# Optimization experiments

Measured on AMD Instinct MI355X. Metric: run time of the kernel, lower is better.

The kernel has to match this reference:

```python
import jax, jax.numpy as jnp
import numpy as np

B, L = 8, 896
D_MODEL, N_HEAD, D_HEAD, D_INNER = 320, 10, 32, 1280
LN_EPS = 1e-5


def layernorm(x, g, b):
    mu = jnp.mean(x, axis=-1, keepdims=True)
    var = jnp.mean(jnp.square(x - mu), axis=-1, keepdims=True)
    return (x - mu) * jax.lax.rsqrt(var + LN_EPS) * g + b


def setup_inputs() -> dict:
    key = jax.random.key(0)
    ks = jax.random.split(key, 8)
    w = lambda k, shape: (jax.random.normal(k, shape, jnp.float32) * 0.02)
    return {
        "Z": jax.random.normal(ks[0], (B, L, D_MODEL), jnp.float32),
        "D": jax.random.uniform(ks[1], (B, L, L), jnp.float32),  # nonneg sq-distance bias
        "new_mask": jnp.zeros((B, L, L), jnp.float32),           # additive mask (0 = keep)
        "mask": jnp.ones((B, L, L), jnp.float32),                # multiplicative validity mask
        "gamma": jnp.ones((4, 4), jnp.float32),
        "w_qkv": w(ks[2], (D_MODEL, 3 * D_MODEL)),
        "b_qkv": jnp.zeros((3 * D_MODEL,), jnp.float32),
        "w_o": w(ks[3], (D_MODEL, D_MODEL)),
        "ln1_g": jnp.ones((D_MODEL,), jnp.float32),
        "ln1_b": jnp.zeros((D_MODEL,), jnp.float32),
        "ln2_g": jnp.ones((D_MODEL,), jnp.float32),
        "ln2_b": jnp.zeros((D_MODEL,), jnp.float32),
        "w1": w(ks[4], (D_MODEL, D_INNER)),
        "b1": jnp.zeros((D_INNER,), jnp.float32),
        "w2": w(ks[5], (D_INNER, D_MODEL)),
        "b2": jnp.zeros((D_MODEL,), jnp.float32),
        "N": 128, "M": 256, "P": 512,
    }


def reference(Z, D, new_mask, mask, gamma, w_qkv, b_qkv, w_o,
              ln1_g, ln1_b, ln2_g, ln2_b, w1, b1, w2, b2, N, M, P):
    bsz, n_elem, _ = Z.shape
    sqrtd = np.sqrt(D_HEAD).astype(np.float32)

    # per-pair type bias: segment ids 0=atom,1=bond,2=triplet (use_quad=False)
    seg = jnp.concatenate([
        jnp.zeros((N,), jnp.int32),
        jnp.ones((M,), jnp.int32),
        jnp.full((P,), 2, jnp.int32),
    ])  # [L]
    gamma_mask = gamma[seg[:, None], seg[None, :]]  # [L, L]

    inp = Z
    Zn = layernorm(Z, ln1_g, ln1_b)
    qkv = (Zn @ w_qkv + b_qkv).reshape(bsz, n_elem, N_HEAD, 3 * D_HEAD)
    Z2, Z3, Z4 = jnp.split(qkv, 3, axis=3)  # each [b, L, h, d]

    # scores [b, h, n, m]
    scores = jnp.einsum('bnhd,bmhd->bhnm', Z3, Z4) / sqrtd
    W = -(gamma_mask[None] * D)[:, None] + scores + new_mask[:, None]
    W = jax.nn.softmax(W, axis=3) * mask[:, None]

    attn_out = jnp.einsum('bhnm,bmhd->bnhd', W, Z2).reshape(bsz, n_elem, D_MODEL)
    attn_out = jax.nn.leaky_relu(attn_out, 0.01) @ w_o  # o_net has no bias
    Z_res = attn_out + inp

    Zn2 = layernorm(Z_res, ln2_g, ln2_b)
    out = jax.nn.relu(Zn2 @ w1 + b1) @ w2 + b2 + Z_res
    return out
```

## Files before the change

kernel.cpp:

```cpp
#include <hip/hip_runtime.h>

#define BB 8
#define LLEN 896
#define DMODEL 320
#define NHEAD 10
#define DHEAD 32
#define DINNER 1280
#define ROWS (BB*LLEN)

typedef float f32x4 __attribute__((ext_vector_type(4)));
typedef float f32x16 __attribute__((ext_vector_type(16)));
typedef __bf16 bf16x8 __attribute__((ext_vector_type(8)));

__device__ __forceinline__ float bf2f(unsigned short u) {
    union { unsigned int i; float f; } x;
    x.i = ((unsigned int)u) << 16;
    return x.f;
}
__device__ __forceinline__ unsigned short f2bf(float f) {
    unsigned int u = __float_as_uint(f);
    u += 0x7FFF + ((u >> 16) & 1);
    return (unsigned short)(u >> 16);
}

#define GLOAD16(g, l)                                                              \
    __builtin_amdgcn_global_load_lds(                                              \
        (const __attribute__((address_space(1))) void*)(g),                        \
        (__attribute__((address_space(3))) void*)(__attribute__((address_space(3))) char*)(l), \
        16, 0, 0)

__global__ __launch_bounds__(256) void transpose_bf16(const float* __restrict__ src,
                                                      unsigned short* __restrict__ dst,
                                                      int R, int C) {
    __shared__ float tile[32][33];
    int c0 = blockIdx.x * 32;
    int r0 = blockIdx.y * 32;
    int tx = threadIdx.x & 31, ty = threadIdx.x >> 5;
#pragma unroll
    for (int k = 0; k < 4; ++k) {
        int yy = ty + 8 * k;
        tile[yy][tx] = src[(size_t)(r0 + yy) * C + c0 + tx];
    }
    __syncthreads();
#pragma unroll
    for (int k = 0; k < 4; ++k) {
        int yy = ty + 8 * k;
        dst[(size_t)(c0 + yy) * R + r0 + tx] = f2bf(tile[tx][yy]);
    }
}

__global__ __launch_bounds__(256) void prepass(const float* __restrict__ D,
                                               const float* __restrict__ nm,
                                               const float* __restrict__ mk,
                                               const float* __restrict__ gamma,
                                               unsigned int* __restrict__ combo) {
    __shared__ unsigned int tile[32][33];
    int mt = blockIdx.x, m0 = mt * 32;
    int n0 = blockIdx.y * 32;
    int b = blockIdx.z;
    int sn = (n0 < 128) ? 0 : (n0 < 384) ? 1 : 2;
    int sm = (m0 < 128) ? 0 : (m0 < 384) ? 1 : 2;
    float g = gamma[sn * 4 + sm];
    int tx = threadIdx.x & 31, ty = threadIdx.x >> 5;
#pragma unroll
    for (int k = 0; k < 4; ++k) {
        int nl = ty + 8 * k;
        size_t idx = ((size_t)b * LLEN + n0 + nl) * LLEN + m0 + tx;
        float bias = -g * D[idx] + nm[idx];
        tile[nl][tx] = (unsigned int)f2bf(bias) | ((unsigned int)f2bf(mk[idx]) << 16);
    }
    __syncthreads();
#pragma unroll
    for (int k = 0; k < 4; ++k) {
        int nl = ty + 8 * k;
        combo[(((size_t)b * 28 + mt) * LLEN + n0 + nl) * 32 + tx] = tile[nl][tx];
    }
}

__global__ __launch_bounds__(256) void vt_kernel(const unsigned short* __restrict__ qkv,
                                                 unsigned short* __restrict__ Vt) {
    __shared__ unsigned short tile[32][33];
    int mt = blockIdx.x, h = blockIdx.y, b = blockIdx.z;
    int tx = threadIdx.x & 31, ty = threadIdx.x >> 5;
#pragma unroll
    for (int k = 0; k < 4; ++k) {
        int ml = ty + 8 * k;
        tile[ml][tx] = qkv[((size_t)(b * LLEN) + mt * 32 + ml) * 960 + h * 96 + tx];
    }
    __syncthreads();
#pragma unroll
    for (int k = 0; k < 4; ++k) {
        int d = ty + 8 * k;
        Vt[(((size_t)b * NHEAD + h) * 32 + d) * LLEN + mt * 32 + tx] = tile[tx][d];
    }
}

__global__ __launch_bounds__(320) void ln_kernel(const float* __restrict__ x,
                                                 const float* __restrict__ g,
                                                 const float* __restrict__ bia,
                                                 unsigned short* __restrict__ y) {
    int row = blockIdx.x;
    int t = threadIdx.x;
    float v = x[(size_t)row * DMODEL + t];
    float s = v;
#pragma unroll
    for (int o = 1; o < 64; o <<= 1) s += __shfl_xor(s, o, 64);
    __shared__ float red[10];
    int w = t >> 6;
    if ((t & 63) == 0) red[w] = s;
    __syncthreads();
    float mu = (red[0] + red[1] + red[2] + red[3] + red[4]) * (1.0f / DMODEL);
    float d = v - mu;
    float s2 = d * d;
#pragma unroll
    for (int o = 1; o < 64; o <<= 1) s2 += __shfl_xor(s2, o, 64);
    if ((t & 63) == 0) red[5 + w] = s2;
    __syncthreads();
    float var = (red[5] + red[6] + red[7] + red[8] + red[9]) * (1.0f / DMODEL);
    float inv = rsqrtf(var + 1e-5f);
    y[(size_t)row * DMODEL + t] = f2bf(d * inv * g[t] + bia[t]);
}

template <int EPI>
__global__ __launch_bounds__(256) void gemm_bt(const unsigned short* __restrict__ A,
                                               const unsigned short* __restrict__ BT,
                                               const float* __restrict__ bias,
                                               const float* __restrict__ resid,
                                               void* __restrict__ outv,
                                               int M, int N, int K) {
    __shared__ unsigned short As[2][128][64];
    __shared__ unsigned short Bs[2][64][64];
    int tid = threadIdx.x;
    int m0 = blockIdx.x * 128;
    int n0 = blockIdx.y * 64;
    int wid = tid >> 6, l = tid & 63;
    int wr = wid >> 1, wc = wid & 1;
    int lr = l & 15, lh = l >> 4;
    int srow = tid >> 3;
    int sslot = (tid & 7) ^ (srow & 7);

    f32x4 acc[4][2];
#pragma unroll
    for (int mi = 0; mi < 4; ++mi)
#pragma unroll
        for (int ni = 0; ni < 2; ++ni) acc[mi][ni] = (f32x4){0.f, 0.f, 0.f, 0.f};

#define STAGE(buf, k0)                                                              \
    {                                                                               \
        _Pragma("unroll")                                                           \
        for (int i = 0; i < 4; ++i)                                                 \
            GLOAD16(&A[(size_t)(m0 + i * 32 + srow) * K + (k0) + sslot * 8],        \
                    (char*)&As[buf][0][0] + i * 4096 + tid * 16);                   \
        _Pragma("unroll")                                                           \
        for (int i = 0; i < 2; ++i)                                                 \
            GLOAD16(&BT[(size_t)(n0 + i * 32 + srow) * K + (k0) + sslot * 8],       \
                    (char*)&Bs[buf][0][0] + i * 4096 + tid * 16);                   \
    }

    int nsteps = K >> 6;
    STAGE(0, 0);
    int cur = 0;
#pragma unroll 1
    for (int t = 0; t < nsteps; ++t) {
        if (t + 1 < nsteps) {
            STAGE(cur ^ 1, (t + 1) * 64);
            asm volatile("s_waitcnt vmcnt(6)" ::: "memory");
        } else {
            asm volatile("s_waitcnt vmcnt(0)" ::: "memory");
        }
        __builtin_amdgcn_s_barrier();
#pragma unroll
        for (int kk = 0; kk < 2; ++kk) {
            int gch = kk * 4 + lh;
            int sl = gch ^ (lr & 7);
            bf16x8 b0 = *(const bf16x8*)&Bs[cur][wc * 32 + lr][sl * 8];
            bf16x8 b1 = *(const bf16x8*)&Bs[cur][wc * 32 + 16 + lr][sl * 8];
#pragma unroll
            for (int mi = 0; mi < 4; ++mi) {
                bf16x8 a = *(const bf16x8*)&As[cur][wr * 64 + mi * 16 + lr][sl * 8];
                acc[mi][0] = __builtin_amdgcn_mfma_f32_16x16x32_bf16(a, b0, acc[mi][0], 0, 0, 0);
                acc[mi][1] = __builtin_amdgcn_mfma_f32_16x16x32_bf16(a, b1, acc[mi][1], 0, 0, 0);
            }
        }
        __builtin_amdgcn_s_barrier();
        cur ^= 1;
    }
#undef STAGE

    unsigned short* outb = (unsigned short*)outv;
    float* outf = (float*)outv;
#pragma unroll
    for (int mi = 0; mi < 4; ++mi)
#pragma unroll
        for (int ni = 0; ni < 2; ++ni) {
            int col = n0 + wc * 32 + ni * 16 + lr;
            float bv = (EPI != 1) ? bias[col] : 0.f;
#pragma unroll
            for (int j = 0; j < 4; ++j) {
                int row = m0 + wr * 64 + mi * 16 + lh * 4 + j;
                float v = acc[mi][ni][j];
                if (EPI == 0 || EPI == 2 || EPI == 3) v += bv;
                if (EPI == 2) v = fmaxf(v, 0.0f);
                if (EPI == 1 || EPI == 3) v += resid[(size_t)row * N + col];
                if (EPI == 0 || EPI == 2) outb[(size_t)row * N + col] = f2bf(v);
                else outf[(size_t)row * N + col] = v;
            }
        }
}

__global__ __launch_bounds__(64) void attn_mfma(const unsigned short* __restrict__ qkv,
                                                const unsigned short* __restrict__ Vt,
                                                const unsigned int* __restrict__ combo,
                                                unsigned short* __restrict__ attn) {
    int l = threadIdx.x;
    int c = l & 31;
    int hi = l >> 5;
    int nt = blockIdx.x % 28;
    int b = blockIdx.x / 28;
    int h = blockIdx.y;
    int n0 = nt * 32;

    size_t qbase = ((size_t)(b * LLEN + n0 + c)) * 960 + h * 96 + 32 + hi * 8;
    bf16x8 qB0 = *(const bf16x8*)&qkv[qbase];
    bf16x8 qB1 = *(const bf16x8*)&qkv[qbase + 16];

    const unsigned int* cbase = combo + ((size_t)b * 28 * LLEN + n0 + c) * 32;
    size_t kbase = (size_t)b * LLEN * 960 + h * 96 + 64 + hi * 8;
    const unsigned short* vrow = Vt + (((size_t)b * NHEAD + h) * 32 + c) * LLEN;

#define ALOAD(mt, K0, K1, V1_, V2_, X4)                                     \
    {                                                                       \
        size_t krow = kbase + (size_t)((mt) * 32 + c) * 960;                \
        K0 = *(const bf16x8*)&qkv[krow];                                    \
        K1 = *(const bf16x8*)&qkv[krow + 16];                               \
        V1_ = *(const bf16x8*)&vrow[(mt) * 32 + hi * 8];                    \
        V2_ = *(const bf16x8*)&vrow[(mt) * 32 + 16 + hi * 8];               \
        const unsigned int* cp = cbase + (size_t)(mt) * (LLEN * 32);        \
        X4[0] = *(const int4*)&cp[4 * hi];                                  \
        X4[1] = *(const int4*)&cp[8 + 4 * hi];                              \
        X4[2] = *(const int4*)&cp[16 + 4 * hi];                             \
        X4[3] = *(const int4*)&cp[24 + 4 * hi];                             \
    }

#define ACOMPUTE(K0, K1, V1_, V2_, X4, OACC, LSUM)                                    \
    {                                                                                 \
        f32x16 sacc = {0.f,0.f,0.f,0.f,0.f,0.f,0.f,0.f,0.f,0.f,0.f,0.f,0.f,0.f,0.f,0.f}; \
        sacc = __builtin_amdgcn_mfma_f32_32x32x16_bf16(K0, qB0, sacc, 0, 0, 0);       \
        sacc = __builtin_amdgcn_mfma_f32_32x32x16_bf16(K1, qB1, sacc, 0, 0, 0);       \
        float p[16];                                                                  \
        _Pragma("unroll")                                                             \
        for (int r = 0; r < 16; ++r) {                                                \
            unsigned int cm = ((const unsigned int*)X4)[r];                           \
            float bias = __uint_as_float(cm << 16);                                   \
            float mk = __uint_as_float(cm & 0xffff0000u);                             \
            float s = fmaf(sacc[r], 0.17677669529663687f, bias);                      \
            float e = __expf(s);                                                      \
            LSUM += e;                                                                \
            p[r] = e * mk;                                                            \
        }                                                                             \
        unsigned int u[8], x[8];                                                      \
        _Pragma("unroll")                                                             \
        for (int j = 0; j < 8; ++j) {                                                 \
            union { __bf16 h2[2]; unsigned int w; } pk;                               \
            pk.h2[0] = (__bf16)p[2 * j];                                              \
            pk.h2[1] = (__bf16)p[2 * j + 1];                                          \
            u[j] = pk.w;                                                              \
            x[j] = (unsigned int)__shfl_xor((int)u[j], 32, 64);                       \
        }                                                                             \
        union { unsigned int w[4]; bf16x8 v; } a1, a2;                                \
        if (hi == 0) {                                                                \
            a1.w[0] = u[0]; a1.w[1] = u[1]; a1.w[2] = x[0]; a1.w[3] = x[1];           \
            a2.w[0] = u[4]; a2.w[1] = u[5]; a2.w[2] = x[4]; a2.w[3] = x[5];           \
        } else {                                                                      \
            a1.w[0] = x[2]; a1.w[1] = x[3]; a1.w[2] = u[2]; a1.w[3] = u[3];           \
            a2.w[0] = x[6]; a2.w[1] = x[7]; a2.w[2] = u[6]; a2.w[3] = u[7];           \
        }                                                                             \
        OACC = __builtin_amdgcn_mfma_f32_32x32x16_bf16(a1.v, V1_, OACC, 0, 0, 0);     \
        OACC = __builtin_amdgcn_mfma_f32_32x32x16_bf16(a2.v, V2_, OACC, 0, 0, 0);     \
    }

    f32x16 oaccA = {0.f,0.f,0.f,0.f,0.f,0.f,0.f,0.f,0.f,0.f,0.f,0.f,0.f,0.f,0.f,0.f};
    f32x16 oaccB = oaccA;
    float lsumA = 0.f, lsumB = 0.f;
    bf16x8 k0A, k1A, v1A, v2A; int4 xA[4];
    bf16x8 k0B, k1B, v1B, v2B; int4 xB[4];
    ALOAD(0, k0A, k1A, v1A, v2A, xA);
    ALOAD(14, k0B, k1B, v1B, v2B, xB);
#pragma unroll 1
    for (int i = 0; i < 14; ++i) {
        ACOMPUTE(k0A, k1A, v1A, v2A, xA, oaccA, lsumA);
        if (i < 13) ALOAD(i + 1, k0A, k1A, v1A, v2A, xA);
        ACOMPUTE(k0B, k1B, v1B, v2B, xB, oaccB, lsumB);
        if (i < 13) ALOAD(i + 15, k0B, k1B, v1B, v2B, xB);
    }
#undef ALOAD
#undef ACOMPUTE

    f32x16 oacc = oaccA + oaccB;
    float lsum = lsumA + lsumB;
    lsum += __shfl_xor(lsum, 32, 64);
    float invs = 1.0f / lsum;
#pragma unroll
    for (int r = 0; r < 16; ++r) {
        int n = (r & 3) + 8 * (r >> 2) + 4 * hi;
        float o = oacc[r] * __shfl(invs, n, 64);
        o = (o >= 0.f) ? o : 0.01f * o;
        attn[((size_t)(b * LLEN + n0 + n)) * DMODEL + h * DHEAD + c] = f2bf(o);
    }
}

extern "C" void kernel_launch(void* const* d_in, const int* in_sizes, int n_in,
                              void* d_out, int out_size, void* d_ws, size_t ws_size,
                              hipStream_t stream) {
    const float* Z     = (const float*)d_in[0];
    const float* Dm    = (const float*)d_in[1];
    const float* nmask = (const float*)d_in[2];
    const float* mask  = (const float*)d_in[3];
    const float* gamma = (const float*)d_in[4];
    const float* w_qkv = (const float*)d_in[5];
    const float* b_qkv = (const float*)d_in[6];
    const float* w_o   = (const float*)d_in[7];
    const float* ln1g  = (const float*)d_in[8];
    const float* ln1b  = (const float*)d_in[9];
    const float* ln2g  = (const float*)d_in[10];
    const float* ln2b  = (const float*)d_in[11];
    const float* w1    = (const float*)d_in[12];
    const float* b1    = (const float*)d_in[13];
    const float* w2    = (const float*)d_in[14];
    const float* b2    = (const float*)d_in[15];

    char* ws = (char*)d_ws;
    unsigned short* Zn    = (unsigned short*)(ws + 0);
    unsigned short* qkv   = (unsigned short*)(ws + 4587520);
    unsigned short* attn  = (unsigned short*)(ws + 18350080);
    float*          Zres  = (float*)(ws + 22937600);
    unsigned short* Zn2   = (unsigned short*)(ws + 32112640);
    unsigned short* Hbuf  = (unsigned short*)(ws + 36700160);
    unsigned short* wqkvT = (unsigned short*)(ws + 55050240);
    unsigned short* woT   = (unsigned short*)(ws + 55664640);
    unsigned short* w1T   = (unsigned short*)(ws + 55869440);
    unsigned short* w2T   = (unsigned short*)(ws + 56688640);
    unsigned int*   combo = (unsigned int*)(ws + 57507840);
    unsigned short* Vtb   = (unsigned short*)(ws + 83197952);

    transpose_bf16<<<dim3(960 / 32, 320 / 32), 256, 0, stream>>>(w_qkv, wqkvT, 320, 960);
    transpose_bf16<<<dim3(320 / 32, 320 / 32), 256, 0, stream>>>(w_o, woT, 320, 320);
    transpose_bf16<<<dim3(1280 / 32, 320 / 32), 256, 0, stream>>>(w1, w1T, 320, 1280);
    transpose_bf16<<<dim3(320 / 32, 1280 / 32), 256, 0, stream>>>(w2, w2T, 1280, 320);

    prepass<<<dim3(28, 28, 8), 256, 0, stream>>>(Dm, nmask, mask, gamma, combo);

    ln_kernel<<<ROWS, 320, 0, stream>>>(Z, ln1g, ln1b, Zn);

    gemm_bt<0><<<dim3(ROWS / 128, 960 / 64), 256, 0, stream>>>(Zn, wqkvT, b_qkv, nullptr,
                                                               (void*)qkv, ROWS, 960, 320);

    vt_kernel<<<dim3(28, NHEAD, BB), 256, 0, stream>>>(qkv, Vtb);

    attn_mfma<<<dim3(BB * 28, NHEAD), 64, 0, stream>>>(qkv, Vtb, combo, attn);

    gemm_bt<1><<<dim3(ROWS / 128, 320 / 64), 256, 0, stream>>>(attn, woT, nullptr, Z,
                                                               (void*)Zres, ROWS, 320, 320);

    ln_kernel<<<ROWS, 320, 0, stream>>>(Zres, ln2g, ln2b, Zn2);

    gemm_bt<2><<<dim3(ROWS / 128, 1280 / 64), 256, 0, stream>>>(Zn2, w1T, b1, nullptr,
                                                                (void*)Hbuf, ROWS, 1280, 320);

    gemm_bt<3><<<dim3(ROWS / 128, 320 / 64), 256, 0, stream>>>(Hbuf, w2T, b2, Zres,
                                                               d_out, ROWS, 320, 1280);
}
```

Baseline: 309.2 us.

## Fuse V transpose into QKV GEMM, merge weight transposes, regroup attention heads

Merges the four weight-transpose launches into one kernel and removes the separate V-transpose kernel. The QKV GEMM epilogue now also writes the transposed V buffer directly. The attention kernel now runs five heads per 320-thread block instead of one head per 64-thread block. It uses exp2f with a log2e-prescaled bias (folded into the prepass) and an inline v_cvt_pk_bf16_f32 for packing. This cuts launch count and an extra pass over qkv, at the cost of scattered 8-byte stores in the GEMM epilogue.

```diff
diff --git a/kernel.cpp b/kernel.cpp
--- a/kernel.cpp
+++ b/kernel.cpp
@@ -29,12 +29,24 @@
         (__attribute__((address_space(3))) void*)(__attribute__((address_space(3))) char*)(l), \
         16, 0, 0)
 
-__global__ __launch_bounds__(256) void transpose_bf16(const float* __restrict__ src,
-                                                      unsigned short* __restrict__ dst,
-                                                      int R, int C) {
+__global__ __launch_bounds__(256) void prep_all(const float* __restrict__ w_qkv,
+                                                const float* __restrict__ w_o,
+                                                const float* __restrict__ w1,
+                                                const float* __restrict__ w2,
+                                                unsigned short* __restrict__ wqkvT,
+                                                unsigned short* __restrict__ woT,
+                                                unsigned short* __restrict__ w1T,
+                                                unsigned short* __restrict__ w2T) {
     __shared__ float tile[32][33];
-    int c0 = blockIdx.x * 32;
-    int r0 = blockIdx.y * 32;
+    int bid = blockIdx.x;
+    const float* src; unsigned short* dst; int R, C, t;
+    if (bid < 300)      { src = w_qkv; dst = wqkvT; R = 320;  C = 960;  t = bid; }
+    else if (bid < 400) { src = w_o;   dst = woT;   R = 320;  C = 320;  t = bid - 300; }
+    else if (bid < 800) { src = w1;    dst = w1T;   R = 320;  C = 1280; t = bid - 400; }
+    else                { src = w2;    dst = w2T;   R = 1280; C = 320;  t = bid - 800; }
+    int tiles_x = C >> 5;
+    int c0 = (t % tiles_x) * 32;
+    int r0 = (t / tiles_x) * 32;
     int tx = threadIdx.x & 31, ty = threadIdx.x >> 5;
 #pragma unroll
     for (int k = 0; k < 4; ++k) {
@@ -66,7 +78,7 @@
     for (int k = 0; k < 4; ++k) {
         int nl = ty + 8 * k;
         size_t idx = ((size_t)b * LLEN + n0 + nl) * LLEN + m0 + tx;
-        float bias = -g * D[idx] + nm[idx];
+        float bias = (-g * D[idx] + nm[idx]) * 1.4426950408889634f;
         tile[nl][tx] = (unsigned int)f2bf(bias) | ((unsigned int)f2bf(mk[idx]) << 16);
     }
     __syncthreads();
@@ -74,24 +86,6 @@
     for (int k = 0; k < 4; ++k) {
         int nl = ty + 8 * k;
         combo[(((size_t)b * 28 + mt) * LLEN + n0 + nl) * 32 + tx] = tile[nl][tx];
-    }
-}
-
-__global__ __launch_bounds__(256) void vt_kernel(const unsigned short* __restrict__ qkv,
-                                                 unsigned short* __restrict__ Vt) {
-    __shared__ unsigned short tile[32][33];
-    int mt = blockIdx.x, h = blockIdx.y, b = blockIdx.z;
-    int tx = threadIdx.x & 31, ty = threadIdx.x >> 5;
-#pragma unroll
-    for (int k = 0; k < 4; ++k) {
-        int ml = ty + 8 * k;
-        tile[ml][tx] = qkv[((size_t)(b * LLEN) + mt * 32 + ml) * 960 + h * 96 + tx];
-    }
-    __syncthreads();
-#pragma unroll
-    for (int k = 0; k < 4; ++k) {
-        int d = ty + 8 * k;
-        Vt[(((size_t)b * NHEAD + h) * 32 + d) * LLEN + mt * 32 + tx] = tile[tx][d];
     }
 }
 
@@ -127,6 +121,7 @@
                                                const float* __restrict__ bias,
                                                const float* __restrict__ resid,
                                                void* __restrict__ outv,
+                                               unsigned short* __restrict__ vtout,
                                                int M, int N, int K) {
     __shared__ unsigned short As[2][128][64];
     __shared__ unsigned short Bs[2][64][64];
@@ -195,6 +190,7 @@
         for (int ni = 0; ni < 2; ++ni) {
             int col = n0 + wc * 32 + ni * 16 + lr;
             float bv = (EPI != 1) ? bias[col] : 0.f;
+            unsigned short vv[4];
 #pragma unroll
             for (int j = 0; j < 4; ++j) {
                 int row = m0 + wr * 64 + mi * 16 + lh * 4 + j;
@@ -202,22 +198,38 @@
                 if (EPI == 0 || EPI == 2 || EPI == 3) v += bv;
                 if (EPI == 2) v = fmaxf(v, 0.0f);
                 if (EPI == 1 || EPI == 3) v += resid[(size_t)row * N + col];
-                if (EPI == 0 || EPI == 2) outb[(size_t)row * N + col] = f2bf(v);
-                else outf[(size_t)row * N + col] = v;
+                if (EPI == 0 || EPI == 2) {
+                    unsigned short ob = f2bf(v);
+                    outb[(size_t)row * N + col] = ob;
+                    vv[j] = ob;
+                } else outf[(size_t)row * N + col] = v;
+            }
+            if (EPI == 0 && vtout) {
+                int cf = n0 + wc * 32 + ni * 16;
+                int h = cf / 96;
+                int d0 = cf - h * 96;
+                if (d0 < 32) {
+                    int b2 = blockIdx.x / 7;
+                    int mf = (blockIdx.x % 7) * 128 + wr * 64 + mi * 16 + lh * 4;
+                    unsigned short* vp =
+                        vtout + (((size_t)b2 * NHEAD + h) * 32 + d0 + lr) * LLEN + mf;
+                    *(ushort4*)vp = *(ushort4*)vv;
+                }
             }
         }
 }
 
-__global__ __launch_bounds__(64) void attn_mfma(const unsigned short* __restrict__ qkv,
-                                                const unsigned short* __restrict__ Vt,
-                                                const unsigned int* __restrict__ combo,
-                                                unsigned short* __restrict__ attn) {
-    int l = threadIdx.x;
+__global__ __launch_bounds__(320) void attn_mfma(const unsigned short* __restrict__ qkv,
+                                                 const unsigned short* __restrict__ Vt,
+                                                 const unsigned int* __restrict__ combo,
+                                                 unsigned short* __restrict__ attn) {
+    int tid = threadIdx.x;
+    int h = blockIdx.x * 5 + (tid >> 6);
+    int l = tid & 63;
     int c = l & 31;
     int hi = l >> 5;
-    int nt = blockIdx.x % 28;
-    int b = blockIdx.x / 28;
-    int h = blockIdx.y;
+    int nt = blockIdx.y % 28;
+    int b = blockIdx.y / 28;
     int n0 = nt * 32;
 
     size_t qbase = ((size_t)(b * LLEN + n0 + c)) * 960 + h * 96 + 32 + hi * 8;
@@ -253,18 +265,15 @@
             unsigned int cm = ((const unsigned int*)X4)[r];                           \
             float bias = __uint_as_float(cm << 16);                                   \
             float mk = __uint_as_float(cm & 0xffff0000u);                             \
-            float s = fmaf(sacc[r], 0.17677669529663687f, bias);                      \
-            float e = __expf(s);                                                      \
+            float e = exp2f(fmaf(sacc[r], 0.25500527f, bias));                        \
             LSUM += e;                                                                \
             p[r] = e * mk;                                                            \
         }                                                                             \
         unsigned int u[8], x[8];                                                      \
         _Pragma("unroll")                                                             \
         for (int j = 0; j < 8; ++j) {                                                 \
-            union { __bf16 h2[2]; unsigned int w; } pk;                               \
-            pk.h2[0] = (__bf16)p[2 * j];                                              \
-            pk.h2[1] = (__bf16)p[2 * j + 1];                                          \
-            u[j] = pk.w;                                                              \
+            asm("v_cvt_pk_bf16_f32 %0, %1, %2"                                        \
+                : "=v"(u[j]) : "v"(p[2 * j]), "v"(p[2 * j + 1]));                     \
             x[j] = (unsigned int)__shfl_xor((int)u[j], 32, 64);                       \
         }                                                                             \
         union { unsigned int w[4]; bf16x8 v; } a1, a2;                                \
@@ -343,30 +352,25 @@
     unsigned int*   combo = (unsigned int*)(ws + 57507840);
     unsigned short* Vtb   = (unsigned short*)(ws + 83197952);
 
-    transpose_bf16<<<dim3(960 / 32, 320 / 32), 256, 0, stream>>>(w_qkv, wqkvT, 320, 960);
-    transpose_bf16<<<dim3(320 / 32, 320 / 32), 256, 0, stream>>>(w_o, woT, 320, 320);
-    transpose_bf16<<<dim3(1280 / 32, 320 / 32), 256, 0, stream>>>(w1, w1T, 320, 1280);
-    transpose_bf16<<<dim3(320 / 32, 1280 / 32), 256, 0, stream>>>(w2, w2T, 1280, 320);
+    prep_all<<<1200, 256, 0, stream>>>(w_qkv, w_o, w1, w2, wqkvT, woT, w1T, w2T);
 
     prepass<<<dim3(28, 28, 8), 256, 0, stream>>>(Dm, nmask, mask, gamma, combo);
 
     ln_kernel<<<ROWS, 320, 0, stream>>>(Z, ln1g, ln1b, Zn);
 
     gemm_bt<0><<<dim3(ROWS / 128, 960 / 64), 256, 0, stream>>>(Zn, wqkvT, b_qkv, nullptr,
-                                                               (void*)qkv, ROWS, 960, 320);
-
-    vt_kernel<<<dim3(28, NHEAD, BB), 256, 0, stream>>>(qkv, Vtb);
-
-    attn_mfma<<<dim3(BB * 28, NHEAD), 64, 0, stream>>>(qkv, Vtb, combo, attn);
+                                                               (void*)qkv, Vtb, ROWS, 960, 320);
+
+    attn_mfma<<<dim3(2, BB * 28), 320, 0, stream>>>(qkv, Vtb, combo, attn);
 
     gemm_bt<1><<<dim3(ROWS / 128, 320 / 64), 256, 0, stream>>>(attn, woT, nullptr, Z,
-                                                               (void*)Zres, ROWS, 320, 320);
+                                                               (void*)Zres, nullptr, ROWS, 320, 320);
 
     ln_kernel<<<ROWS, 320, 0, stream>>>(Zres, ln2g, ln2b, Zn2);
 
     gemm_bt<2><<<dim3(ROWS / 128, 1280 / 64), 256, 0, stream>>>(Zn2, w1T, b1, nullptr,
-                                                                (void*)Hbuf, ROWS, 1280, 320);
+                                                                (void*)Hbuf, nullptr, ROWS, 1280, 320);
 
     gemm_bt<3><<<dim3(ROWS / 128, 320 / 64), 256, 0, stream>>>(Hbuf, w2T, b2, Zres,
-                                                               d_out, ROWS, 320, 1280);
-}
+                                                               d_out, nullptr, ROWS, 320, 1280);
+}
```

Measured after the change: 298.2 us. 1.04x faster.
